# Kernel optimization log

Hardware: AMD Instinct MI355X
Metric: run time of the kernel (lower is better)

The kernel has to match this reference:

```python
import jax, jax.numpy as jnp
import numpy as np

WS = (2, 7, 7)          # window size (Wd, Wh, Ww)
SS = (1, 3, 3)          # shift size
DIM = 96
HEADS = 3
HD = DIM // HEADS       # head dim = 32
N = WS[0] * WS[1] * WS[2]  # 98 tokens per window
EPS = 1e-5


def _rel_index():
    c = np.stack(np.meshgrid(np.arange(WS[0]), np.arange(WS[1]), np.arange(WS[2]), indexing='ij')).reshape(3, -1)
    r = (c[:, :, None] - c[:, None, :]).transpose(1, 2, 0)  # (N, N, 3)
    r[..., 0] += WS[0] - 1
    r[..., 1] += WS[1] - 1
    r[..., 2] += WS[2] - 1
    r[..., 0] *= (2 * WS[1] - 1) * (2 * WS[2] - 1)
    r[..., 1] *= 2 * WS[2] - 1
    return jnp.asarray(r.sum(-1))  # (N, N) int

REL_IDX = _rel_index()


def _ln(x, w, b):
    m = x.mean(-1, keepdims=True)
    v = ((x - m) ** 2).mean(-1, keepdims=True)
    return (x - m) * jax.lax.rsqrt(v + EPS) * w + b


def setup_inputs() -> dict:
    key = jax.random.key(0)
    ks = jax.random.split(key, 10)
    B, D, H, W, C = 2, 16, 112, 112, DIM
    nW = (D // WS[0]) * (H // WS[1]) * (W // WS[2])  # 2048
    s = 0.02
    tbl = (2 * WS[0] - 1) * (2 * WS[1] - 1) * (2 * WS[2] - 1)
    return dict(
        x=jax.random.normal(ks[0], (B, D, H, W, C), jnp.float32),
        mask=jax.random.normal(ks[1], (nW, N, N), jnp.float32),
        norm1_w=jnp.ones((C,), jnp.float32), norm1_b=jnp.zeros((C,), jnp.float32),
        qkv_w=jax.random.normal(ks[2], (C, 3 * C), jnp.float32) * s,
        qkv_b=jnp.zeros((3 * C,), jnp.float32),
        rpb_table=jax.random.normal(ks[3], (tbl, HEADS), jnp.float32) * s,
        proj_w=jax.random.normal(ks[4], (C, C), jnp.float32) * s,
        proj_b=jnp.zeros((C,), jnp.float32),
        norm2_w=jnp.ones((C,), jnp.float32), norm2_b=jnp.zeros((C,), jnp.float32),
        fc1_w=jax.random.normal(ks[5], (C, 4 * C), jnp.float32) * s,
        fc1_b=jnp.zeros((4 * C,), jnp.float32),
        fc2_w=jax.random.normal(ks[6], (4 * C, C), jnp.float32) * s,
        fc2_b=jnp.zeros((C,), jnp.float32),
    )


def reference(x, mask, norm1_w, norm1_b, qkv_w, qkv_b, rpb_table, proj_w, proj_b,
              norm2_w, norm2_b, fc1_w, fc1_b, fc2_w, fc2_b):
    B, D, H, W, C = x.shape
    shortcut = x
    x = _ln(x, norm1_w, norm1_b)
    # shift (dims divisible by window -> no padding needed)
    x = jnp.roll(x, shift=(-SS[0], -SS[1], -SS[2]), axis=(1, 2, 3))
    nd, nh, nw = D // WS[0], H // WS[1], W // WS[2]
    # window partition -> (B*nW, N, C)
    xw = x.reshape(B, nd, WS[0], nh, WS[1], nw, WS[2], C)
    xw = xw.transpose(0, 1, 3, 5, 2, 4, 6, 7).reshape(-1, N, C)
    B_ = xw.shape[0]
    qkv = (xw @ qkv_w + qkv_b).reshape(B_, N, 3, HEADS, HD).transpose(2, 0, 3, 1, 4)
    q, k, v = qkv[0] * (HD ** -0.5), qkv[1], qkv[2]
    attn = jnp.einsum('bhnd,bhmd->bhnm', q, k)  # (B_, H, N, N)
    bias = rpb_table[REL_IDX.reshape(-1)].reshape(N, N, HEADS).transpose(2, 0, 1)
    attn = attn + bias[None]
    nWm = mask.shape[0]
    attn = attn.reshape(B_ // nWm, nWm, HEADS, N, N) + mask[None, :, None]
    attn = jax.nn.softmax(attn.reshape(B_, HEADS, N, N), axis=-1)
    out = jnp.einsum('bhnm,bhmd->bhnd', attn, v).transpose(0, 2, 1, 3).reshape(B_, N, C)
    out = out @ proj_w + proj_b
    # window reverse
    x = out.reshape(B, nd, nh, nw, WS[0], WS[1], WS[2], C)
    x = x.transpose(0, 1, 4, 2, 5, 3, 6, 7).reshape(B, D, H, W, C)
    x = jnp.roll(x, shift=SS, axis=(1, 2, 3))
    x = shortcut + x
    y = _ln(x, norm2_w, norm2_b)
    y = jax.nn.gelu(y @ fc1_w + fc1_b, approximate=False) @ fc2_w + fc2_b
    return x + y
```

## Files before the change

### kernel.cpp

```cpp
#include <hip/hip_runtime.h>

typedef float f32x4 __attribute__((ext_vector_type(4)));
typedef __bf16 bf16x8 __attribute__((ext_vector_type(8)));
typedef unsigned short ushort_t;
typedef ushort_t us4 __attribute__((ext_vector_type(4)));
typedef unsigned int u32x4 __attribute__((ext_vector_type(4)));

#define MFMA16(a, b, c) __builtin_amdgcn_mfma_f32_16x16x32_bf16((a), (b), (c), 0, 0, 0)

__device__ __forceinline__ ushort_t f2bf(float f) {
    unsigned int u = __builtin_bit_cast(unsigned int, f);
    u += 0x7fffu + ((u >> 16) & 1u);
    return (ushort_t)(u >> 16);
}
__device__ __forceinline__ float bf2f(ushort_t u) {
    return __builtin_bit_cast(float, (unsigned int)u << 16);
}
__device__ __forceinline__ unsigned int packbf2(float lo, float hi) {
    return ((unsigned int)f2bf(hi) << 16) | (unsigned int)f2bf(lo);
}

__device__ __forceinline__ float gelu_fast(float x) {
    float x2 = x * x;
    float t = __builtin_fmaf(0.044715f * x2, x, x);
    float e = __builtin_amdgcn_exp2f(t * (-1.5957691216f * 1.44269504f));
    return x * __builtin_amdgcn_rcpf(1.0f + e);
}

#define NTOK 98
#define CCH 96
#define QSCALE 0.17677669529663687f

#define WQKVP_OFF   ((size_t)0)
#define WPROJP_OFF  (WQKVP_OFF + (size_t)27648 * 2)
#define WFC1P_OFF   (WPROJP_OFF + (size_t)9216 * 2)
#define WFC2P_OFF   (WFC1P_OFF + (size_t)36864 * 2)
#define BIAS2_OFF   (WFC2P_OFF + (size_t)36864 * 2)
#define MASK2_OFF   (BIAS2_OFF + (size_t)37632 * 2 + 256)

__global__ __launch_bounds__(256) void prep_kernel(
    const float* __restrict__ qkv_w, const float* __restrict__ proj_w,
    const float* __restrict__ fc1_w, const float* __restrict__ fc2_w,
    const float* __restrict__ rpb,
    ushort_t* __restrict__ wqkvP, ushort_t* __restrict__ wprojP,
    ushort_t* __restrict__ wfc1P, ushort_t* __restrict__ wfc2P,
    ushort_t* __restrict__ bias2)
{
    int i = blockIdx.x * 256 + threadIdx.x;
    if (i < 27648) {
        int f = i >> 9, r = i & 511, lane = r >> 3, m = r & 7;
        int k0 = f % 3, t = f / 3, nt = t % 2, t2 = t / 2, w = t2 % 3, h = t2 / 3;
        int row = k0 * 32 + (lane >> 4) * 8 + m;
        int col = w * 96 + h * 32 + nt * 16 + (lane & 15);
        wqkvP[i] = f2bf(qkv_w[row * 288 + col]);
        return;
    }
    i -= 27648;
    if (i < 9216) {
        int f = i >> 9, r = i & 511, lane = r >> 3, m = r & 7;
        int k0 = f % 3, nt = f / 3;
        int row = k0 * 32 + (lane >> 4) * 8 + m;
        int col = nt * 16 + (lane & 15);
        wprojP[i] = f2bf(proj_w[row * 96 + col]);
        return;
    }
    i -= 9216;
    if (i < 36864) {
        int f = i >> 9, r = i & 511, lane = r >> 3, m = r & 7;
        int k0 = f % 3, nt = f / 3;
        int row = k0 * 32 + (lane >> 4) * 8 + m;
        int col = nt * 16 + (lane & 15);
        wfc1P[i] = f2bf(fc1_w[row * 384 + col]);
        return;
    }
    i -= 36864;
    if (i < 36864) {
        int f = i >> 9, r = i & 511, lane = r >> 3, m = r & 7;
        int k0 = f % 12, nt = f / 12;
        int row = k0 * 32 + (lane >> 4) * 8 + m;
        int col = nt * 16 + (lane & 15);
        wfc2P[i] = f2bf(fc2_w[row * 96 + col]);
        return;
    }
    i -= 36864;
    if (i < 37632) {
        int h = i / 12544, rem = i % 12544;
        int mt = rem / 1792, rem2 = rem % 1792, kc = rem2 >> 4, r16 = rem2 & 15;
        int row = mt * 16 + r16;
        float v = 0.f;
        if (row < 98 && kc < 98) {
            int rd = row / 49 - kc / 49 + 1;
            int rh = (row % 49) / 7 - (kc % 49) / 7 + 6;
            int rw = row % 7 - kc % 7 + 6;
            v = rpb[((rd * 13 + rh) * 13 + rw) * 3 + h];
        }
        bias2[i] = f2bf(v);
    }
}

__global__ __launch_bounds__(256) void mask2_kernel(
    const float* __restrict__ mask, ushort_t* __restrict__ mask2)
{
    __shared__ float m_lds[9604];
    const int wm = blockIdx.x;
    const float* mw = mask + (size_t)wm * 9604;
    for (int i = threadIdx.x; i < 9604; i += 256) m_lds[i] = mw[i];
    __syncthreads();
    ushort_t* out = mask2 + (size_t)wm * 12544;
    for (int g = threadIdx.x; g < 3136; g += 256) {
        int mt = g / 448, rem = g % 448, kc = rem >> 2, r4 = (rem & 3) * 4;
        us4 o;
        #pragma unroll
        for (int e = 0; e < 4; ++e) {
            int row = mt * 16 + r4 + e;
            float v = (row < 98 && kc < 98) ? m_lds[row * 98 + kc] : -1e30f;
            o[e] = f2bf(v);
        }
        *(us4*)(out + (size_t)g * 4) = o;
    }
}

__global__ __launch_bounds__(192, 3) void fused_attn(
    const float* __restrict__ x, const ushort_t* __restrict__ mask2,
    const float* __restrict__ n1w, const float* __restrict__ n1b,
    const float* __restrict__ qkv_b, const float* __restrict__ proj_b,
    const ushort_t* __restrict__ wqkvP, const ushort_t* __restrict__ wprojP,
    const ushort_t* __restrict__ bias2, float* __restrict__ dout)
{
    __shared__ ushort_t xw_lds[112 * 104];
    __shared__ ushort_t sc_all[3][2176];
    __shared__ int tokbase[112];

    const int tid  = threadIdx.x;
    const int lane = tid & 63;
    const int wave = tid >> 6;
    const int l16  = lane & 15, lg = lane >> 4;

    const int b  = blockIdx.x;
    const int wm = (b & 7) * 256 + ((b >> 3) >> 1);
    const int bb = (b >> 3) & 1;
    const int id_ = wm >> 8, ih = (wm >> 4) & 15, iw = wm & 15;

    if (tid < 98) {
        int td = tid / 49, r49 = tid - td * 49, th = r49 / 7, tw = r49 - th * 7;
        int od = (id_ * 2 + td + 1) & 15;
        int oh = ih * 7 + th + 3; if (oh >= 112) oh -= 112;
        int ow = iw * 7 + tw + 3; if (ow >= 112) ow -= 112;
        tokbase[tid] = ((((bb << 4) + od) * 112 + oh) * 112 + ow) * 96;
    }
    {
        us4 z4 = {0, 0, 0, 0};
        for (int i = tid; i < 14 * 26; i += 192) {
            int t = 98 + i / 26, c4 = (i % 26) * 4;
            *(us4*)(xw_lds + t * 104 + c4) = z4;
        }
    }
    __syncthreads();

    {
        const int g = tid >> 5, lane32 = tid & 31;
        for (int t = g; t < 98; t += 6) {
            const float* xp = x + tokbase[t];
            float v0 = xp[lane32], v1 = xp[lane32 + 32], v2 = xp[lane32 + 64];
            float s = v0 + v1 + v2, sq = v0 * v0 + v1 * v1 + v2 * v2;
            #pragma unroll
            for (int m = 1; m < 32; m <<= 1) { s += __shfl_xor(s, m); sq += __shfl_xor(sq, m); }
            float mean = s * (1.0f / 96.0f);
            float var = sq * (1.0f / 96.0f) - mean * mean;
            float rs = rsqrtf(var + 1e-5f);
            ushort_t* op = xw_lds + t * 104;
            op[lane32]      = f2bf((v0 - mean) * rs * n1w[lane32]      + n1b[lane32]);
            op[lane32 + 32] = f2bf((v1 - mean) * rs * n1w[lane32 + 32] + n1b[lane32 + 32]);
            op[lane32 + 64] = f2bf((v2 - mean) * rs * n1w[lane32 + 64] + n1b[lane32 + 64]);
        }
    }
    __syncthreads();

    const int h = wave;
    ushort_t* sc = sc_all[wave];
    const ushort_t* m2w = mask2 + (size_t)wm * 12544;
    const ushort_t* b2h = bias2 + (size_t)h * 12544;

    bf16x8 qf[7], kf[7], vf[2][4];

    #pragma unroll
    for (int which = 0; which < 2; ++which) {
        bf16x8 bw[2][3];
        float  bia[2];
        #pragma unroll
        for (int nt = 0; nt < 2; ++nt) {
            bia[nt] = qkv_b[which * 96 + h * 32 + nt * 16 + l16];
            #pragma unroll
            for (int k0 = 0; k0 < 3; ++k0)
                bw[nt][k0] = *(const bf16x8*)(wqkvP + ((((h * 3 + which) * 2 + nt) * 3 + k0) << 9) + lane * 8);
        }
        for (int mt = 0; mt < 7; ++mt) {
            const ushort_t* ap = xw_lds + (mt * 16 + l16) * 104 + lg * 8;
            bf16x8 a0 = *(const bf16x8*)(ap);
            bf16x8 a1 = *(const bf16x8*)(ap + 32);
            bf16x8 a2 = *(const bf16x8*)(ap + 64);
            #pragma unroll
            for (int nt = 0; nt < 2; ++nt) {
                f32x4 acc = {0.f, 0.f, 0.f, 0.f};
                acc = MFMA16(a0, bw[nt][0], acc);
                acc = MFMA16(a1, bw[nt][1], acc);
                acc = MFMA16(a2, bw[nt][2], acc);
                float scl = (which == 0) ? QSCALE : 1.0f;
                #pragma unroll
                for (int j = 0; j < 4; ++j)
                    sc[(lg * 4 + j) * 36 + nt * 16 + l16] = f2bf((acc[j] + bia[nt]) * scl);
            }
            if (which == 0) qf[mt] = *(const bf16x8*)(sc + l16 * 36 + lg * 8);
            else            kf[mt] = *(const bf16x8*)(sc + l16 * 36 + lg * 8);
        }
    }

    {
        bf16x8 bw[2][3];
        float  bia[2];
        #pragma unroll
        for (int nt = 0; nt < 2; ++nt) {
            bia[nt] = qkv_b[192 + h * 32 + nt * 16 + l16];
            #pragma unroll
            for (int k0 = 0; k0 < 3; ++k0)
                bw[nt][k0] = *(const bf16x8*)(wqkvP + ((((h * 3 + 2) * 2 + nt) * 3 + k0) << 9) + lane * 8);
        }
        #pragma unroll
        for (int k0 = 0; k0 < 4; ++k0) {
            unsigned int pkv[2][2][2];
            #pragma unroll
            for (int half = 0; half < 2; ++half) {
                int mtp = 2 * k0 + half;
                if (mtp < 7) {
                    const ushort_t* ap = xw_lds + (mtp * 16 + l16) * 104 + lg * 8;
                    bf16x8 a0 = *(const bf16x8*)(ap);
                    bf16x8 a1 = *(const bf16x8*)(ap + 32);
                    bf16x8 a2 = *(const bf16x8*)(ap + 64);
                    #pragma unroll
                    for (int nt2 = 0; nt2 < 2; ++nt2) {
                        f32x4 acc = {0.f, 0.f, 0.f, 0.f};
                        acc = MFMA16(a0, bw[nt2][0], acc);
                        acc = MFMA16(a1, bw[nt2][1], acc);
                        acc = MFMA16(a2, bw[nt2][2], acc);
                        pkv[half][nt2][0] = packbf2(acc[0] + bia[nt2], acc[1] + bia[nt2]);
                        pkv[half][nt2][1] = packbf2(acc[2] + bia[nt2], acc[3] + bia[nt2]);
                    }
                } else {
                    pkv[half][0][0] = pkv[half][0][1] = 0u;
                    pkv[half][1][0] = pkv[half][1][1] = 0u;
                }
            }
            #pragma unroll
            for (int nt2 = 0; nt2 < 2; ++nt2) {
                u32x4 w;
                #pragma unroll
                for (int e = 0; e < 4; ++e) {
                    int s = l16 + 16 * (2 * (lg & 1) + (e >> 1));
                    unsigned int t0 = (unsigned int)__shfl((int)pkv[0][nt2][e & 1], s, 64);
                    unsigned int t1 = (unsigned int)__shfl((int)pkv[1][nt2][e & 1], s, 64);
                    w[e] = (lg >> 1) ? t1 : t0;
                }
                vf[nt2][k0] = __builtin_bit_cast(bf16x8, w);
            }
        }
    }
    __syncthreads();

    ushort_t* out = xw_lds;

    if (lane < 32) {
        us4 z4 = {0, 0, 0, 0};
        *(us4*)(sc + (lane >> 1) * 136 + 112 + (lane & 1) * 8) = z4;
        *(us4*)(sc + (lane >> 1) * 136 + 116 + (lane & 1) * 8) = z4;
    }

    #pragma unroll
    for (int mt = 0; mt < 7; ++mt) {
        const ushort_t* m2t = m2w + mt * 1792;
        const ushort_t* b2t = b2h + mt * 1792;
        us4 mv[7];
        #pragma unroll
        for (int nt = 0; nt < 7; ++nt)
            mv[nt] = *(const us4*)(m2t + (nt * 16 + l16) * 16 + lg * 4);

        f32x4 sums = {0.f, 0.f, 0.f, 0.f};
        #pragma unroll
        for (int nt = 0; nt < 7; ++nt) {
            us4 bv = *(const us4*)(b2t + (nt * 16 + l16) * 16 + lg * 4);
            f32x4 z = {0.f, 0.f, 0.f, 0.f};
            f32x4 stv = MFMA16(qf[mt], kf[nt], z);
            #pragma unroll
            for (int j = 0; j < 4; ++j) {
                float e_ = __expf(stv[j] + bf2f(mv[nt][j]) + bf2f(bv[j]));
                sums[j] += e_;
                sc[(lg * 4 + j) * 136 + nt * 16 + l16] = f2bf(e_);
            }
        }
        f32x4 inv;
        #pragma unroll
        for (int j = 0; j < 4; ++j) {
            float s = sums[j];
            s += __shfl_xor(s, 1); s += __shfl_xor(s, 2);
            s += __shfl_xor(s, 4); s += __shfl_xor(s, 8);
            inv[j] = __builtin_amdgcn_rcpf(s);
        }
        bf16x8 pf[4];
        #pragma unroll
        for (int k0 = 0; k0 < 4; ++k0)
            pf[k0] = *(const bf16x8*)(sc + l16 * 136 + k0 * 32 + lg * 8);
        #pragma unroll
        for (int nt2 = 0; nt2 < 2; ++nt2) {
            f32x4 acc = {0.f, 0.f, 0.f, 0.f};
            #pragma unroll
            for (int k0 = 0; k0 < 4; ++k0) acc = MFMA16(pf[k0], vf[nt2][k0], acc);
            #pragma unroll
            for (int j = 0; j < 4; ++j) {
                int tok = mt * 16 + lg * 4 + j;
                if (tok < 98)
                    out[tok * 104 + h * 32 + nt2 * 16 + l16] = f2bf(acc[j] * inv[j]);
            }
        }
    }
    __syncthreads();

    for (int job = wave; job < 42; job += 3) {
        int mt = job / 6, nt = job % 6;
        int cg = nt * 16 + l16;
        f32x4 acc = {0.f, 0.f, 0.f, 0.f};
        #pragma unroll
        for (int k0 = 0; k0 < 3; ++k0) {
            bf16x8 ao = *(const bf16x8*)(out + (mt * 16 + l16) * 104 + k0 * 32 + lg * 8);
            bf16x8 bp = *(const bf16x8*)(wprojP + ((nt * 3 + k0) << 9) + lane * 8);
            acc = MFMA16(ao, bp, acc);
        }
        float pb = proj_b[cg];
        #pragma unroll
        for (int j = 0; j < 4; ++j) {
            int tok = mt * 16 + lg * 4 + j;
            if (tok < 98) {
                int g = tokbase[tok] + cg;
                dout[g] = x[g] + acc[j] + pb;
            }
        }
    }
}

__global__ __launch_bounds__(256, 5) void mlp_kernel(
    float* __restrict__ xres, const float* __restrict__ w2, const float* __restrict__ b2,
    const ushort_t* __restrict__ wfc1P, const float* __restrict__ fc1_b,
    const ushort_t* __restrict__ wfc2P, const float* __restrict__ fc2_b)
{
    __shared__ ushort_t A_ln[32 * 104];
    __shared__ ushort_t h_lds[32 * 392];
    const int tid = threadIdx.x;
    const int lane = tid & 63, wave = tid >> 6;
    const int l16 = lane & 15, lg = lane >> 4;
    const size_t t0 = (size_t)blockIdx.x * 32;

    {
        int t = tid >> 3, sub = tid & 7;
        const float* xp = xres + (t0 + t) * 96;
        f32x4 v[3];
        float s = 0.f, sq = 0.f;
        #pragma unroll
        for (int j4 = 0; j4 < 3; ++j4) {
            v[j4] = *(const f32x4*)(xp + (j4 * 8 + sub) * 4);
            #pragma unroll
            for (int e = 0; e < 4; ++e) { s += v[j4][e]; sq += v[j4][e] * v[j4][e]; }
        }
        s += __shfl_xor(s, 1); s += __shfl_xor(s, 2); s += __shfl_xor(s, 4);
        sq += __shfl_xor(sq, 1); sq += __shfl_xor(sq, 2); sq += __shfl_xor(sq, 4);
        float mean = s * (1.0f / 96.0f);
        float var = sq * (1.0f / 96.0f) - mean * mean;
        float rs = rsqrtf(var + 1e-5f);
        #pragma unroll
        for (int j4 = 0; j4 < 3; ++j4) {
            int c0 = (j4 * 8 + sub) * 4;
            us4 pk;
            #pragma unroll
            for (int e = 0; e < 4; ++e)
                pk[e] = f2bf((v[j4][e] - mean) * rs * w2[c0 + e] + b2[c0 + e]);
            *(us4*)(A_ln + t * 104 + c0) = pk;
        }
    }
    __syncthreads();

    for (int job = wave; job < 48; job += 4) {
        int mt = job / 24, nt = job % 24;
        int n = nt * 16 + l16;
        f32x4 acc = {0.f, 0.f, 0.f, 0.f};
        #pragma unroll
        for (int k0 = 0; k0 < 3; ++k0) {
            bf16x8 a  = *(const bf16x8*)(A_ln + (mt * 16 + l16) * 104 + k0 * 32 + lg * 8);
            bf16x8 bw = *(const bf16x8*)(wfc1P + ((nt * 3 + k0) << 9) + lane * 8);
            acc = MFMA16(a, bw, acc);
        }
        float bv = fc1_b[n];
        #pragma unroll
        for (int j = 0; j < 4; ++j) {
            int tok = mt * 16 + lg * 4 + j;
            h_lds[tok * 392 + n] = f2bf(gelu_fast(acc[j] + bv));
        }
    }
    __syncthreads();

    for (int job = wave; job < 12; job += 4) {
        int mt = job / 6, nt = job % 6;
        int c = nt * 16 + l16;
        f32x4 acc = {0.f, 0.f, 0.f, 0.f};
        #pragma unroll
        for (int k0 = 0; k0 < 12; ++k0) {
            bf16x8 a  = *(const bf16x8*)(h_lds + (mt * 16 + l16) * 392 + k0 * 32 + lg * 8);
            bf16x8 bw = *(const bf16x8*)(wfc2P + ((nt * 12 + k0) << 9) + lane * 8);
            acc = MFMA16(a, bw, acc);
        }
        float bv = fc2_b[c];
        #pragma unroll
        for (int j = 0; j < 4; ++j) {
            int tok = mt * 16 + lg * 4 + j;
            size_t g = (t0 + tok) * 96 + c;
            xres[g] = xres[g] + acc[j] + bv;
        }
    }
}

extern "C" void kernel_launch(void* const* d_in, const int* in_sizes, int n_in,
                              void* d_out, int out_size, void* d_ws, size_t ws_size,
                              hipStream_t stream) {
    const float* x      = (const float*)d_in[0];
    const float* mask   = (const float*)d_in[1];
    const float* n1w    = (const float*)d_in[2];
    const float* n1b    = (const float*)d_in[3];
    const float* qkv_w  = (const float*)d_in[4];
    const float* qkv_b  = (const float*)d_in[5];
    const float* rpb    = (const float*)d_in[6];
    const float* proj_w = (const float*)d_in[7];
    const float* proj_b = (const float*)d_in[8];
    const float* n2w    = (const float*)d_in[9];
    const float* n2b    = (const float*)d_in[10];
    const float* fc1_w  = (const float*)d_in[11];
    const float* fc1_b  = (const float*)d_in[12];
    const float* fc2_w  = (const float*)d_in[13];
    const float* fc2_b  = (const float*)d_in[14];

    char* ws = (char*)d_ws;
    ushort_t* wqkvP  = (ushort_t*)(ws + WQKVP_OFF);
    ushort_t* wprojP = (ushort_t*)(ws + WPROJP_OFF);
    ushort_t* wfc1P  = (ushort_t*)(ws + WFC1P_OFF);
    ushort_t* wfc2P  = (ushort_t*)(ws + WFC2P_OFF);
    ushort_t* bias2  = (ushort_t*)(ws + BIAS2_OFF);
    ushort_t* mask2  = (ushort_t*)(ws + MASK2_OFF);
    float*    dout   = (float*)d_out;

    prep_kernel<<<579, 256, 0, stream>>>(qkv_w, proj_w, fc1_w, fc2_w, rpb,
                                         wqkvP, wprojP, wfc1P, wfc2P, bias2);
    mask2_kernel<<<2048, 256, 0, stream>>>(mask, mask2);
    fused_attn<<<4096, 192, 0, stream>>>(x, mask2, n1w, n1b, qkv_b, proj_b,
                                         wqkvP, wprojP, bias2, dout);
    mlp_kernel<<<12544, 256, 0, stream>>>(dout, n2w, n2b, wfc1P, fc1_b, wfc2P, fc2_b);
}
```

Baseline: 497.5 us.

## Fuse MLP into windowed attention kernel and switch softmax to exp2

The separate MLP kernel is removed, and each attention block now runs LayerNorm2, FC1 with GELU, FC2 and the residual add on its own 98 window tokens, reusing LDS buffers. The goal is to drop the global round trip of the intermediate activations and one kernel launch. As a second change, the bias, mask and Q scale are premultiplied by log2(e) so the softmax can call the native exp2. The cost is that the three-wave block now does the MLP work with per-row-tile syncs and less parallelism than the old 256-thread MLP kernel. It also depends on hbuf fitting inside sc_all (16x392 shorts against 3x2176), which looks tight.

```diff
diff --git a/kernel.cpp b/kernel.cpp
--- a/kernel.cpp
+++ b/kernel.cpp
@@ -7,6 +7,7 @@
 typedef unsigned int u32x4 __attribute__((ext_vector_type(4)));
 
 #define MFMA16(a, b, c) __builtin_amdgcn_mfma_f32_16x16x32_bf16((a), (b), (c), 0, 0, 0)
+#define LOG2E 1.4426950408889634f
 
 __device__ __forceinline__ ushort_t f2bf(float f) {
     unsigned int u = __builtin_bit_cast(unsigned int, f);
@@ -92,7 +93,7 @@
             int rd = row / 49 - kc / 49 + 1;
             int rh = (row % 49) / 7 - (kc % 49) / 7 + 6;
             int rw = row % 7 - kc % 7 + 6;
-            v = rpb[((rd * 13 + rh) * 13 + rw) * 3 + h];
+            v = rpb[((rd * 13 + rh) * 13 + rw) * 3 + h] * LOG2E;
         }
         bias2[i] = f2bf(v);
     }
@@ -113,19 +114,23 @@
         #pragma unroll
         for (int e = 0; e < 4; ++e) {
             int row = mt * 16 + r4 + e;
-            float v = (row < 98 && kc < 98) ? m_lds[row * 98 + kc] : -1e30f;
+            float v = (row < 98 && kc < 98) ? m_lds[row * 98 + kc] * LOG2E : -1e30f;
             o[e] = f2bf(v);
         }
         *(us4*)(out + (size_t)g * 4) = o;
     }
 }
 
-__global__ __launch_bounds__(192, 3) void fused_attn(
+__global__ __launch_bounds__(192, 3) void fused_block(
     const float* __restrict__ x, const ushort_t* __restrict__ mask2,
     const float* __restrict__ n1w, const float* __restrict__ n1b,
     const float* __restrict__ qkv_b, const float* __restrict__ proj_b,
     const ushort_t* __restrict__ wqkvP, const ushort_t* __restrict__ wprojP,
-    const ushort_t* __restrict__ bias2, float* __restrict__ dout)
+    const ushort_t* __restrict__ bias2,
+    const float* __restrict__ n2w, const float* __restrict__ n2b,
+    const ushort_t* __restrict__ wfc1P, const float* __restrict__ fc1_b,
+    const ushort_t* __restrict__ wfc2P, const float* __restrict__ fc2_b,
+    float* __restrict__ dout)
 {
     __shared__ ushort_t xw_lds[112 * 104];
     __shared__ ushort_t sc_all[3][2176];
@@ -205,7 +210,7 @@
                 acc = MFMA16(a0, bw[nt][0], acc);
                 acc = MFMA16(a1, bw[nt][1], acc);
                 acc = MFMA16(a2, bw[nt][2], acc);
-                float scl = (which == 0) ? QSCALE : 1.0f;
+                float scl = (which == 0) ? (QSCALE * LOG2E) : 1.0f;
                 #pragma unroll
                 for (int j = 0; j < 4; ++j)
                     sc[(lg * 4 + j) * 36 + nt * 16 + l16] = f2bf((acc[j] + bia[nt]) * scl);
@@ -291,7 +296,7 @@
             f32x4 stv = MFMA16(qf[mt], kf[nt], z);
             #pragma unroll
             for (int j = 0; j < 4; ++j) {
-                float e_ = __expf(stv[j] + bf2f(mv[nt][j]) + bf2f(bv[j]));
+                float e_ = __builtin_amdgcn_exp2f(stv[j] + bf2f(mv[nt][j]) + bf2f(bv[j]));
                 sums[j] += e_;
                 sc[(lg * 4 + j) * 136 + nt * 16 + l16] = f2bf(e_);
             }
@@ -343,84 +348,65 @@
             }
         }
     }
-}
-
-__global__ __launch_bounds__(256, 5) void mlp_kernel(
-    float* __restrict__ xres, const float* __restrict__ w2, const float* __restrict__ b2,
-    const ushort_t* __restrict__ wfc1P, const float* __restrict__ fc1_b,
-    const ushort_t* __restrict__ wfc2P, const float* __restrict__ fc2_b)
-{
-    __shared__ ushort_t A_ln[32 * 104];
-    __shared__ ushort_t h_lds[32 * 392];
-    const int tid = threadIdx.x;
-    const int lane = tid & 63, wave = tid >> 6;
-    const int l16 = lane & 15, lg = lane >> 4;
-    const size_t t0 = (size_t)blockIdx.x * 32;
+    __syncthreads();
 
     {
-        int t = tid >> 3, sub = tid & 7;
-        const float* xp = xres + (t0 + t) * 96;
-        f32x4 v[3];
-        float s = 0.f, sq = 0.f;
-        #pragma unroll
-        for (int j4 = 0; j4 < 3; ++j4) {
-            v[j4] = *(const f32x4*)(xp + (j4 * 8 + sub) * 4);
-            #pragma unroll
-            for (int e = 0; e < 4; ++e) { s += v[j4][e]; sq += v[j4][e] * v[j4][e]; }
-        }
-        s += __shfl_xor(s, 1); s += __shfl_xor(s, 2); s += __shfl_xor(s, 4);
-        sq += __shfl_xor(sq, 1); sq += __shfl_xor(sq, 2); sq += __shfl_xor(sq, 4);
-        float mean = s * (1.0f / 96.0f);
-        float var = sq * (1.0f / 96.0f) - mean * mean;
-        float rs = rsqrtf(var + 1e-5f);
-        #pragma unroll
-        for (int j4 = 0; j4 < 3; ++j4) {
-            int c0 = (j4 * 8 + sub) * 4;
-            us4 pk;
-            #pragma unroll
-            for (int e = 0; e < 4; ++e)
-                pk[e] = f2bf((v[j4][e] - mean) * rs * w2[c0 + e] + b2[c0 + e]);
-            *(us4*)(A_ln + t * 104 + c0) = pk;
-        }
-    }
-    __syncthreads();
-
-    for (int job = wave; job < 48; job += 4) {
-        int mt = job / 24, nt = job % 24;
-        int n = nt * 16 + l16;
-        f32x4 acc = {0.f, 0.f, 0.f, 0.f};
-        #pragma unroll
-        for (int k0 = 0; k0 < 3; ++k0) {
-            bf16x8 a  = *(const bf16x8*)(A_ln + (mt * 16 + l16) * 104 + k0 * 32 + lg * 8);
-            bf16x8 bw = *(const bf16x8*)(wfc1P + ((nt * 3 + k0) << 9) + lane * 8);
-            acc = MFMA16(a, bw, acc);
-        }
-        float bv = fc1_b[n];
-        #pragma unroll
-        for (int j = 0; j < 4; ++j) {
-            int tok = mt * 16 + lg * 4 + j;
-            h_lds[tok * 392 + n] = f2bf(gelu_fast(acc[j] + bv));
-        }
-    }
-    __syncthreads();
-
-    for (int job = wave; job < 12; job += 4) {
-        int mt = job / 6, nt = job % 6;
-        int c = nt * 16 + l16;
-        f32x4 acc = {0.f, 0.f, 0.f, 0.f};
-        #pragma unroll
-        for (int k0 = 0; k0 < 12; ++k0) {
-            bf16x8 a  = *(const bf16x8*)(h_lds + (mt * 16 + l16) * 392 + k0 * 32 + lg * 8);
-            bf16x8 bw = *(const bf16x8*)(wfc2P + ((nt * 12 + k0) << 9) + lane * 8);
-            acc = MFMA16(a, bw, acc);
-        }
-        float bv = fc2_b[c];
-        #pragma unroll
-        for (int j = 0; j < 4; ++j) {
-            int tok = mt * 16 + lg * 4 + j;
-            size_t g = (t0 + tok) * 96 + c;
-            xres[g] = xres[g] + acc[j] + bv;
-        }
+        const int g = tid >> 5, lane32 = tid & 31;
+        for (int t = g; t < 98; t += 6) {
+            const float* xp = dout + tokbase[t];
+            float v0 = xp[lane32], v1 = xp[lane32 + 32], v2 = xp[lane32 + 64];
+            float s = v0 + v1 + v2, sq = v0 * v0 + v1 * v1 + v2 * v2;
+            #pragma unroll
+            for (int m = 1; m < 32; m <<= 1) { s += __shfl_xor(s, m); sq += __shfl_xor(sq, m); }
+            float mean = s * (1.0f / 96.0f);
+            float var = sq * (1.0f / 96.0f) - mean * mean;
+            float rs = rsqrtf(var + 1e-5f);
+            ushort_t* op = xw_lds + t * 104;
+            op[lane32]      = f2bf((v0 - mean) * rs * n2w[lane32]      + n2b[lane32]);
+            op[lane32 + 32] = f2bf((v1 - mean) * rs * n2w[lane32 + 32] + n2b[lane32 + 32]);
+            op[lane32 + 64] = f2bf((v2 - mean) * rs * n2w[lane32 + 64] + n2b[lane32 + 64]);
+        }
+    }
+    ushort_t* hbuf = &sc_all[0][0];
+    __syncthreads();
+
+    for (int mt = 0; mt < 7; ++mt) {
+        const ushort_t* arow = xw_lds + (mt * 16 + l16) * 104 + lg * 8;
+        bf16x8 a0 = *(const bf16x8*)(arow);
+        bf16x8 a1 = *(const bf16x8*)(arow + 32);
+        bf16x8 a2 = *(const bf16x8*)(arow + 64);
+        for (int nt = wave; nt < 24; nt += 3) {
+            int n = nt * 16 + l16;
+            f32x4 acc = {0.f, 0.f, 0.f, 0.f};
+            acc = MFMA16(a0, *(const bf16x8*)(wfc1P + ((nt * 3 + 0) << 9) + lane * 8), acc);
+            acc = MFMA16(a1, *(const bf16x8*)(wfc1P + ((nt * 3 + 1) << 9) + lane * 8), acc);
+            acc = MFMA16(a2, *(const bf16x8*)(wfc1P + ((nt * 3 + 2) << 9) + lane * 8), acc);
+            float bv = fc1_b[n];
+            #pragma unroll
+            for (int j = 0; j < 4; ++j)
+                hbuf[(lg * 4 + j) * 392 + n] = f2bf(gelu_fast(acc[j] + bv));
+        }
+        __syncthreads();
+        for (int nt = wave; nt < 6; nt += 3) {
+            int c = nt * 16 + l16;
+            f32x4 acc = {0.f, 0.f, 0.f, 0.f};
+            #pragma unroll
+            for (int k0 = 0; k0 < 12; ++k0) {
+                bf16x8 ha = *(const bf16x8*)(hbuf + l16 * 392 + k0 * 32 + lg * 8);
+                bf16x8 bw2 = *(const bf16x8*)(wfc2P + ((nt * 12 + k0) << 9) + lane * 8);
+                acc = MFMA16(ha, bw2, acc);
+            }
+            float bv = fc2_b[c];
+            #pragma unroll
+            for (int j = 0; j < 4; ++j) {
+                int tok = mt * 16 + lg * 4 + j;
+                if (tok < 98) {
+                    int g = tokbase[tok] + c;
+                    dout[g] = dout[g] + acc[j] + bv;
+                }
+            }
+        }
+        __syncthreads();
     }
 }
 
@@ -455,7 +441,7 @@
     prep_kernel<<<579, 256, 0, stream>>>(qkv_w, proj_w, fc1_w, fc2_w, rpb,
                                          wqkvP, wprojP, wfc1P, wfc2P, bias2);
     mask2_kernel<<<2048, 256, 0, stream>>>(mask, mask2);
-    fused_attn<<<4096, 192, 0, stream>>>(x, mask2, n1w, n1b, qkv_b, proj_b,
-                                         wqkvP, wprojP, bias2, dout);
-    mlp_kernel<<<12544, 256, 0, stream>>>(dout, n2w, n2b, wfc1P, fc1_b, wfc2P, fc2_b);
-}
+    fused_block<<<4096, 192, 0, stream>>>(x, mask2, n1w, n1b, qkv_b, proj_b,
+                                          wqkvP, wprojP, bias2,
+                                          n2w, n2b, wfc1P, fc1_b, wfc2P, fc2_b, dout);
+}
```

Measured after the change: 624.1 us. 1.25x slower.
